# Performance work log

Measured on AMD Instinct MI355X. Metric: run time of the kernel, lower is better.

The kernel has to match this reference:

```python
import jax, jax.numpy as jnp
import numpy as np

EMB = 1024
HID = 1024
VOCAB = 32000
SEQ = 128


def _lstm_cell(x, h, c, W_ih, W_hh, b_ih, b_hh):
    # PyTorch gate order: input, forget, cell(g), output
    gates = x @ W_ih.T + b_ih + h @ W_hh.T + b_hh  # [4H]
    i, f, g, o = jnp.split(gates, 4)
    c_new = jax.nn.sigmoid(f) * c + jax.nn.sigmoid(i) * jnp.tanh(g)
    h_new = jax.nn.sigmoid(o) * jnp.tanh(c_new)
    return h_new, c_new


def setup_inputs() -> dict:
    key = jax.random.key(0)
    ks = jax.random.split(key, 12)
    s_emb = 0.02
    s_lstm = 1.0 / np.sqrt(HID)
    return {
        "sentence": jax.random.randint(ks[0], (SEQ,), 0, VOCAB),
        "given_num": 64,
        "emb": jax.random.normal(ks[1], (VOCAB, EMB), jnp.float32) * s_emb,
        "W_ih_lstm": jax.random.normal(ks[2], (4 * HID, EMB), jnp.float32) * s_lstm,
        "W_hh_lstm": jax.random.normal(ks[3], (4 * HID, HID), jnp.float32) * s_lstm,
        "b_ih_lstm": jax.random.normal(ks[4], (4 * HID,), jnp.float32) * s_lstm,
        "b_hh_lstm": jax.random.normal(ks[5], (4 * HID,), jnp.float32) * s_lstm,
        "W_ih_cell": jax.random.normal(ks[6], (4 * HID, EMB), jnp.float32) * s_lstm,
        "W_hh_cell": jax.random.normal(ks[7], (4 * HID, HID), jnp.float32) * s_lstm,
        "b_ih_cell": jax.random.normal(ks[8], (4 * HID,), jnp.float32) * s_lstm,
        "b_hh_cell": jax.random.normal(ks[9], (4 * HID,), jnp.float32) * s_lstm,
        "W_tag": jax.random.normal(ks[10], (VOCAB, HID), jnp.float32) * s_lstm,
        "b_tag": jax.random.normal(ks[11], (VOCAB,), jnp.float32) * s_lstm,
    }


def reference(sentence, given_num, emb, W_ih_lstm, W_hh_lstm, b_ih_lstm, b_hh_lstm,
              W_ih_cell, W_hh_cell, b_ih_cell, b_hh_cell, W_tag, b_tag):
    given_num = int(given_num)  # static (batch-1 rollout, fixed split point)

    # ---- teacher-forced prefix through nn.LSTM (init_hidden -> zeros) ----
    embeds_existing = emb[sentence[:given_num]]  # [g, E]

    def prefix_step(carry, x):
        h, c = carry
        h, c = _lstm_cell(x, h, c, W_ih_lstm, W_hh_lstm, b_ih_lstm, b_hh_lstm)
        return (h, c), h

    h0 = jnp.zeros((HID,), embeds_existing.dtype)
    (h, c), lstm_out = jax.lax.scan(prefix_step, (h0, h0), embeds_existing)
    tag_prefix = lstm_out @ W_tag.T + b_tag  # [g, V]

    # multinomial over softmax(tag) == categorical over logits; only last row's
    # sample is consumed as x_t
    skeys = jax.random.split(jax.random.key(123), SEQ - given_num + 1)
    x_t = jax.random.categorical(skeys[0], tag_prefix[-1])

    def rollout_step(carry, k):
        x_t, h, c = carry
        e = emb[x_t]
        h, c = _lstm_cell(e, h, c, W_ih_cell, W_hh_cell, b_ih_cell, b_hh_cell)
        logits = h @ W_tag.T + b_tag  # [V]
        x_next = jax.random.categorical(k, logits)
        return (x_next, h, c), logits

    _, tag_roll = jax.lax.scan(rollout_step, (x_t, h, c), skeys[1:])  # [S-g, V]

    tag_space = jnp.concatenate([tag_prefix, tag_roll], axis=0)  # [S, V]
    return jax.nn.log_softmax(tag_space, axis=-1)
```

## Files before the change

kernel.cpp:

```cpp
#include <hip/hip_runtime.h>
#include <cstdint>
#include <cstddef>

#define EMBD 1024
#define HIDD 1024
#define G4   4096
#define VOC  32000
#define SEQL 128
#define GN   64
#define NR   64

#define JAX_PARTITIONABLE 1

__device__ __forceinline__ uint32_t rotl32(uint32_t v, int d) { return (v << d) | (v >> (32 - d)); }

__device__ inline void threefry2x32(uint32_t k0, uint32_t k1, uint32_t x0, uint32_t x1,
                                    uint32_t& o0, uint32_t& o1) {
  uint32_t ks2 = k0 ^ k1 ^ 0x1BD11BDAu;
#define TF_ROUND(r) { x0 += x1; x1 = rotl32(x1, r); x1 ^= x0; }
  x0 += k0;  x1 += k1;
  TF_ROUND(13) TF_ROUND(15) TF_ROUND(26) TF_ROUND(6)
  x0 += k1;  x1 += ks2 + 1u;
  TF_ROUND(17) TF_ROUND(29) TF_ROUND(16) TF_ROUND(24)
  x0 += ks2; x1 += k0 + 2u;
  TF_ROUND(13) TF_ROUND(15) TF_ROUND(26) TF_ROUND(6)
  x0 += k0;  x1 += k1 + 3u;
  TF_ROUND(17) TF_ROUND(29) TF_ROUND(16) TF_ROUND(24)
  x0 += k1;  x1 += ks2 + 4u;
  TF_ROUND(13) TF_ROUND(15) TF_ROUND(26) TF_ROUND(6)
  x0 += ks2; x1 += k0 + 5u;
#undef TF_ROUND
  o0 = x0; o1 = x1;
}

__device__ inline uint32_t rng_bits(uint32_t k0, uint32_t k1, uint32_t idx) {
#if JAX_PARTITIONABLE
  uint32_t h0, h1; threefry2x32(k0, k1, 0u, idx, h0, h1);
  return h0 ^ h1;
#else
  uint32_t h0, h1;
  if (idx < (VOC / 2)) { threefry2x32(k0, k1, idx, idx + (VOC / 2), h0, h1); return h0; }
  else                 { threefry2x32(k0, k1, idx - (VOC / 2), idx, h0, h1); return h1; }
#endif
}

__device__ inline float gumbel_of(uint32_t k0, uint32_t k1, uint32_t idx) {
  uint32_t bits = rng_bits(k0, k1, idx);
  float u = __uint_as_float((bits >> 9) | 0x3f800000u) - 1.0f;
  u = fmaxf(u, 1.17549435e-38f);
  return -logf(-logf(u));
}

__device__ inline unsigned long long packCand(float v, int idx) {
  uint32_t u = __float_as_uint(v);
  u = (u & 0x80000000u) ? ~u : (u | 0x80000000u);
  return ((unsigned long long)u << 32) | (unsigned long long)(0xFFFFFFFFu - (uint32_t)idx);
}

__device__ inline float sigf(float x) { return 1.0f / (1.0f + expf(-x)); }

__global__ void k_init(uint2* keys, unsigned* counters, float* cbuf, float* h0) {
  int t = threadIdx.x;
#if JAX_PARTITIONABLE
  if (t < NR + 1) {
    uint32_t a, b; threefry2x32(0u, 123u, 0u, (uint32_t)t, a, b);
    keys[t] = make_uint2(a, b);
  }
#else
  __shared__ uint32_t buf[2 * (NR + 1)];
  if (t < NR + 1) {
    uint32_t a, b; threefry2x32(0u, 123u, (uint32_t)t, (uint32_t)(t + NR + 1), a, b);
    buf[t] = a; buf[t + NR + 1] = b;
  }
  __syncthreads();
  if (t < NR + 1) keys[t] = make_uint2(buf[2 * t], buf[2 * t + 1]);
#endif
  for (int i = t; i < 66; i += 256) counters[i] = 0u;
  for (int i = t; i < HIDD; i += 256) { cbuf[i] = 0.0f; h0[i] = 0.0f; }
}

__global__ void k_gather(const float* __restrict__ emb, const int* __restrict__ sent,
                         float* __restrict__ X) {
  int m = blockIdx.x;
  int row = sent[m];
  const float4* s = (const float4*)(emb + (size_t)row * EMBD);
  float4* d = (float4*)(X + (size_t)m * EMBD);
  d[threadIdx.x] = s[threadIdx.x];
}

__global__ __launch_bounds__(256) void k_gemm64(const float* __restrict__ A,
                                                const float* __restrict__ B,
                                                const float* __restrict__ bias,
                                                float* __restrict__ C, int ldc) {
  __shared__ float As[64][33];
  __shared__ float Bs[64][33];
  int n0 = blockIdx.x * 64;
  int tn = threadIdx.x & 15, tm = threadIdx.x >> 4;
  float acc[4][4] = {{0.f}};
  for (int k0 = 0; k0 < 1024; k0 += 32) {
    for (int f = threadIdx.x; f < 512; f += 256) {
      int r = f >> 3, c4 = (f & 7) << 2;
      float4 v = *(const float4*)(A + (size_t)r * 1024 + k0 + c4);
      As[r][c4 + 0] = v.x; As[r][c4 + 1] = v.y; As[r][c4 + 2] = v.z; As[r][c4 + 3] = v.w;
      float4 u = *(const float4*)(B + (size_t)(n0 + r) * 1024 + k0 + c4);
      Bs[r][c4 + 0] = u.x; Bs[r][c4 + 1] = u.y; Bs[r][c4 + 2] = u.z; Bs[r][c4 + 3] = u.w;
    }
    __syncthreads();
#pragma unroll
    for (int kk = 0; kk < 32; ++kk) {
      float a0 = As[tm * 4 + 0][kk], a1 = As[tm * 4 + 1][kk];
      float a2 = As[tm * 4 + 2][kk], a3 = As[tm * 4 + 3][kk];
      float b0 = Bs[tn * 4 + 0][kk], b1 = Bs[tn * 4 + 1][kk];
      float b2 = Bs[tn * 4 + 2][kk], b3 = Bs[tn * 4 + 3][kk];
      acc[0][0] += a0 * b0; acc[0][1] += a0 * b1; acc[0][2] += a0 * b2; acc[0][3] += a0 * b3;
      acc[1][0] += a1 * b0; acc[1][1] += a1 * b1; acc[1][2] += a1 * b2; acc[1][3] += a1 * b3;
      acc[2][0] += a2 * b0; acc[2][1] += a2 * b1; acc[2][2] += a2 * b2; acc[2][3] += a2 * b3;
      acc[3][0] += a3 * b0; acc[3][1] += a3 * b1; acc[3][2] += a3 * b2; acc[3][3] += a3 * b3;
    }
    __syncthreads();
  }
#pragma unroll
  for (int i = 0; i < 4; ++i)
#pragma unroll
    for (int j = 0; j < 4; ++j) {
      int m = tm * 4 + i, n = n0 + tn * 4 + j;
      float r = acc[i][j] + (bias ? bias[n] : 0.0f);
      C[(size_t)m * ldc + n] = r;
    }
}

__global__ __launch_bounds__(256) void k_lstm_pre(const float* __restrict__ Whh,
                                                  const float* __restrict__ bih,
                                                  const float* __restrict__ bhh,
                                                  const float* __restrict__ gx, int t,
                                                  const float* __restrict__ hprev,
                                                  float* __restrict__ cbuf,
                                                  float* __restrict__ hout) {
  __shared__ float gs[4];
  int wave = threadIdx.x >> 6, lane = threadIdx.x & 63;
  int j = blockIdx.x;
  int r = j + (wave << 10);
  const float4* h4 = (const float4*)hprev;
  const float4* w4 = (const float4*)(Whh + (size_t)r * 1024);
  float a = 0.0f;
#pragma unroll
  for (int q = 0; q < 4; ++q) {
    float4 w = w4[lane + (q << 6)];
    float4 h = h4[lane + (q << 6)];
    a += w.x * h.x + w.y * h.y + w.z * h.z + w.w * h.w;
  }
#pragma unroll
  for (int off = 32; off; off >>= 1) a += __shfl_xor(a, off, 64);
  if (lane == 0) gs[wave] = a + gx[(size_t)t * G4 + r] + bih[r] + bhh[r];
  __syncthreads();
  if (threadIdx.x == 0) {
    float gi = gs[0], gf = gs[1], gg = gs[2], go = gs[3];
    float cn = sigf(gf) * cbuf[j] + sigf(gi) * tanhf(gg);
    cbuf[j] = cn;
    hout[j] = sigf(go) * tanhf(cn);
  }
}

__global__ __launch_bounds__(256) void k_lstm_roll(const float* __restrict__ Wih,
                                                   const float* __restrict__ Whh,
                                                   const float* __restrict__ bih,
                                                   const float* __restrict__ bhh,
                                                   const float* __restrict__ emb,
                                                   const int* __restrict__ tok, int t,
                                                   const float* __restrict__ hprev,
                                                   float* __restrict__ cbuf,
                                                   float* __restrict__ hout) {
  __shared__ float gs[4];
  int wave = threadIdx.x >> 6, lane = threadIdx.x & 63;
  int j = blockIdx.x;
  int r = j + (wave << 10);
  int row = tok[t];
  const float4* x4 = (const float4*)(emb + (size_t)row * EMBD);
  const float4* h4 = (const float4*)hprev;
  const float4* wi = (const float4*)(Wih + (size_t)r * 1024);
  const float4* wh = (const float4*)(Whh + (size_t)r * 1024);
  float a = 0.0f;
#pragma unroll
  for (int q = 0; q < 4; ++q) {
    float4 w = wi[lane + (q << 6)];
    float4 x = x4[lane + (q << 6)];
    a += w.x * x.x + w.y * x.y + w.z * x.z + w.w * x.w;
    w = wh[lane + (q << 6)];
    float4 h = h4[lane + (q << 6)];
    a += w.x * h.x + w.y * h.y + w.z * h.z + w.w * h.w;
  }
#pragma unroll
  for (int off = 32; off; off >>= 1) a += __shfl_xor(a, off, 64);
  if (lane == 0) gs[wave] = a + bih[r] + bhh[r];
  __syncthreads();
  if (threadIdx.x == 0) {
    float gi = gs[0], gf = gs[1], gg = gs[2], go = gs[3];
    float cn = sigf(gf) * cbuf[j] + sigf(gi) * tanhf(gg);
    cbuf[j] = cn;
    hout[j] = sigf(go) * tanhf(cn);
  }
}

__global__ __launch_bounds__(256) void k_logits(const float* __restrict__ Wtag,
                                                const float* __restrict__ btag,
                                                const float* __restrict__ h,
                                                float* __restrict__ outrow,
                                                const uint2* __restrict__ keys, int key_idx,
                                                unsigned long long* __restrict__ partials,
                                                unsigned* __restrict__ counter,
                                                int* __restrict__ token_out) {
  __shared__ float sums[64];
  __shared__ unsigned long long red[256];
  __shared__ int amLast;
  int wave = threadIdx.x >> 6, lane = threadIdx.x & 63;
  int r0 = blockIdx.x * 64;
  const float4* h4 = (const float4*)h;
  float4 hv[4];
#pragma unroll
  for (int q = 0; q < 4; ++q) hv[q] = h4[lane + (q << 6)];
  for (int rr = 0; rr < 16; ++rr) {
    int lr = wave * 16 + rr;
    int r = r0 + lr;
    const float4* w4 = (const float4*)(Wtag + (size_t)r * 1024);
    float a = 0.0f;
#pragma unroll
    for (int q = 0; q < 4; ++q) {
      float4 w = w4[lane + (q << 6)];
      a += w.x * hv[q].x + w.y * hv[q].y + w.z * hv[q].z + w.w * hv[q].w;
    }
#pragma unroll
    for (int off = 32; off; off >>= 1) a += __shfl_xor(a, off, 64);
    if (lane == 0) sums[lr] = a;
  }
  __syncthreads();
  unsigned long long best = 0ull;
  if (threadIdx.x < 64) {
    int r = r0 + threadIdx.x;
    float L = sums[threadIdx.x] + btag[r];
    outrow[r] = L;
    uint2 K = keys[key_idx];
    float y = L + gumbel_of(K.x, K.y, (uint32_t)r);
    best = packCand(y, r);
#pragma unroll
    for (int off = 32; off; off >>= 1) {
      unsigned long long o = __shfl_xor(best, off, 64);
      if (o > best) best = o;
    }
    if (threadIdx.x == 0) partials[blockIdx.x] = best;
  }
  __threadfence();
  __syncthreads();
  if (threadIdx.x == 0) amLast = (atomicAdd(counter, 1u) == gridDim.x - 1) ? 1 : 0;
  __syncthreads();
  if (amLast) {
    __threadfence();
    unsigned long long b = 0ull;
    for (int i = threadIdx.x; i < (int)gridDim.x; i += 256) {
      unsigned long long v = *((volatile unsigned long long*)(partials + i));
      if (v > b) b = v;
    }
    red[threadIdx.x] = b;
    __syncthreads();
    for (int s = 128; s; s >>= 1) {
      if (threadIdx.x < s) {
        if (red[threadIdx.x + s] > red[threadIdx.x]) red[threadIdx.x] = red[threadIdx.x + s];
      }
      __syncthreads();
    }
    if (threadIdx.x == 0)
      token_out[0] = (int)(0xFFFFFFFFu - (uint32_t)(red[0] & 0xFFFFFFFFull));
  }
}

__global__ __launch_bounds__(256) void k_sample_row(const float* __restrict__ row,
                                                    const uint2* __restrict__ keys, int key_idx,
                                                    unsigned long long* __restrict__ partials,
                                                    unsigned* __restrict__ counter,
                                                    int* __restrict__ token_out) {
  __shared__ unsigned long long red[256];
  __shared__ int amLast;
  int v = blockIdx.x * 256 + threadIdx.x;
  unsigned long long best = 0ull;
  if (v < VOC) {
    uint2 K = keys[key_idx];
    float y = row[v] + gumbel_of(K.x, K.y, (uint32_t)v);
    best = packCand(y, v);
  }
  red[threadIdx.x] = best;
  __syncthreads();
  for (int s = 128; s; s >>= 1) {
    if (threadIdx.x < s) {
      if (red[threadIdx.x + s] > red[threadIdx.x]) red[threadIdx.x] = red[threadIdx.x + s];
    }
    __syncthreads();
  }
  if (threadIdx.x == 0) partials[blockIdx.x] = red[0];
  __threadfence();
  __syncthreads();
  if (threadIdx.x == 0) amLast = (atomicAdd(counter, 1u) == gridDim.x - 1) ? 1 : 0;
  __syncthreads();
  if (amLast) {
    __threadfence();
    unsigned long long b = 0ull;
    for (int i = threadIdx.x; i < (int)gridDim.x; i += 256) {
      unsigned long long val = *((volatile unsigned long long*)(partials + i));
      if (val > b) b = val;
    }
    red[threadIdx.x] = b;
    __syncthreads();
    for (int s = 128; s; s >>= 1) {
      if (threadIdx.x < s) {
        if (red[threadIdx.x + s] > red[threadIdx.x]) red[threadIdx.x] = red[threadIdx.x + s];
      }
      __syncthreads();
    }
    if (threadIdx.x == 0)
      token_out[0] = (int)(0xFFFFFFFFu - (uint32_t)(red[0] & 0xFFFFFFFFull));
  }
}

__global__ __launch_bounds__(256) void k_logsoftmax(float* __restrict__ C) {
  __shared__ float red[256];
  float* row = C + (size_t)blockIdx.x * VOC;
  float m = -INFINITY;
  for (int i = threadIdx.x; i < VOC; i += 256) m = fmaxf(m, row[i]);
  red[threadIdx.x] = m;
  __syncthreads();
  for (int s = 128; s; s >>= 1) {
    if (threadIdx.x < s) red[threadIdx.x] = fmaxf(red[threadIdx.x], red[threadIdx.x + s]);
    __syncthreads();
  }
  m = red[0];
  __syncthreads();
  float sum = 0.0f;
  for (int i = threadIdx.x; i < VOC; i += 256) sum += expf(row[i] - m);
  red[threadIdx.x] = sum;
  __syncthreads();
  for (int s = 128; s; s >>= 1) {
    if (threadIdx.x < s) red[threadIdx.x] += red[threadIdx.x + s];
    __syncthreads();
  }
  float lse = m + logf(red[0]);
  __syncthreads();
  for (int i = threadIdx.x; i < VOC; i += 256) row[i] = row[i] - lse;
}

extern "C" void kernel_launch(void* const* d_in, const int* in_sizes, int n_in,
                              void* d_out, int out_size, void* d_ws, size_t ws_size,
                              hipStream_t stream) {
  (void)in_sizes; (void)n_in; (void)out_size; (void)ws_size;
  const int*   sent  = (const int*)  d_in[0];
  const float* emb   = (const float*)d_in[2];
  const float* Wih_l = (const float*)d_in[3];
  const float* Whh_l = (const float*)d_in[4];
  const float* bih_l = (const float*)d_in[5];
  const float* bhh_l = (const float*)d_in[6];
  const float* Wih_c = (const float*)d_in[7];
  const float* Whh_c = (const float*)d_in[8];
  const float* bih_c = (const float*)d_in[9];
  const float* bhh_c = (const float*)d_in[10];
  const float* Wtag  = (const float*)d_in[11];
  const float* btag  = (const float*)d_in[12];
  float* out = (float*)d_out;

  char* ws = (char*)d_ws;
  uint2*              keys     = (uint2*)(ws + 0);
  int*                tokens   = (int*)(ws + 1024);
  unsigned*           counters = (unsigned*)(ws + 2048);
  unsigned long long* partials = (unsigned long long*)(ws + 4096);
  float*              cbuf     = (float*)(ws + 8192);
  float*              h0       = (float*)(ws + 12288);
  float*              lstm_out = (float*)(ws + 16384);
  float*              hroll    = (float*)(ws + 16384 + 262144);
  float*              X        = (float*)(ws + 16384 + 2 * 262144);
  float*              gx       = (float*)(ws + 16384 + 3 * 262144);

  k_init<<<1, 256, 0, stream>>>(keys, counters, cbuf, h0);
  k_gather<<<GN, 256, 0, stream>>>(emb, sent, X);
  k_gemm64<<<G4 / 64, 256, 0, stream>>>(X, Wih_l, nullptr, gx, G4);
  for (int t = 0; t < GN; ++t) {
    const float* hp = t ? (lstm_out + (size_t)(t - 1) * HIDD) : h0;
    k_lstm_pre<<<HIDD, 256, 0, stream>>>(Whh_l, bih_l, bhh_l, gx, t, hp, cbuf,
                                         lstm_out + (size_t)t * HIDD);
  }
  k_gemm64<<<VOC / 64, 256, 0, stream>>>(lstm_out, Wtag, btag, out, VOC);
  k_sample_row<<<(VOC + 255) / 256, 256, 0, stream>>>(out + (size_t)(GN - 1) * VOC, keys, 0,
                                                      partials, counters + 64, tokens);
  for (int t = 0; t < NR; ++t) {
    const float* hp = t ? (hroll + (size_t)(t - 1) * HIDD) : (lstm_out + (size_t)(GN - 1) * HIDD);
    k_lstm_roll<<<HIDD, 256, 0, stream>>>(Wih_c, Whh_c, bih_c, bhh_c, emb, tokens, t, hp, cbuf,
                                          hroll + (size_t)t * HIDD);
    k_logits<<<VOC / 64, 256, 0, stream>>>(Wtag, btag, hroll + (size_t)t * HIDD,
                                           out + (size_t)(GN + t) * VOC, keys, 1 + t,
                                           partials, counters + t, tokens + t + 1);
  }
  k_logsoftmax<<<SEQL, 256, 0, stream>>>(out);
}
```

Baseline: 5.319 ms.

## Fuse rollout LSTM cell, logits and sampling into one kernel per step

Each rollout step now runs as a single kernel instead of separate LSTM-cell and logits kernels. The first 256 blocks compute the gate pre-activations and signal completion through an atomic counter. All blocks spin until that counter is full, then each recomputes the cell update redundantly into shared memory and computes its slice of the vocabulary logits, Gumbel sample and argmax reduction. The h/c state is double-buffered across steps. The GEMM tile is also narrowed to 32 columns to launch more blocks; the spin barrier relies on all producer blocks being co-resident on the GPU.

```diff
diff --git a/kernel.cpp b/kernel.cpp
--- a/kernel.cpp
+++ b/kernel.cpp
@@ -9,6 +9,8 @@
 #define SEQL 128
 #define GN   64
 #define NR   64
+#define RGRID 500
+#define PPROD 256
 
 #define JAX_PARTITIONABLE 1
 
@@ -61,21 +63,11 @@
 
 __global__ void k_init(uint2* keys, unsigned* counters, float* cbuf, float* h0) {
   int t = threadIdx.x;
-#if JAX_PARTITIONABLE
   if (t < NR + 1) {
     uint32_t a, b; threefry2x32(0u, 123u, 0u, (uint32_t)t, a, b);
     keys[t] = make_uint2(a, b);
   }
-#else
-  __shared__ uint32_t buf[2 * (NR + 1)];
-  if (t < NR + 1) {
-    uint32_t a, b; threefry2x32(0u, 123u, (uint32_t)t, (uint32_t)(t + NR + 1), a, b);
-    buf[t] = a; buf[t + NR + 1] = b;
-  }
-  __syncthreads();
-  if (t < NR + 1) keys[t] = make_uint2(buf[2 * t], buf[2 * t + 1]);
-#endif
-  for (int i = t; i < 66; i += 256) counters[i] = 0u;
+  if (t < 192) counters[t] = 0u;
   for (int i = t; i < HIDD; i += 256) { cbuf[i] = 0.0f; h0[i] = 0.0f; }
 }
 
@@ -88,20 +80,24 @@
   d[threadIdx.x] = s[threadIdx.x];
 }
 
-__global__ __launch_bounds__(256) void k_gemm64(const float* __restrict__ A,
-                                                const float* __restrict__ B,
-                                                const float* __restrict__ bias,
-                                                float* __restrict__ C, int ldc) {
+__global__ __launch_bounds__(256) void k_gemm_n32(const float* __restrict__ A,
+                                                  const float* __restrict__ B,
+                                                  const float* __restrict__ bias,
+                                                  float* __restrict__ C, int ldc) {
   __shared__ float As[64][33];
-  __shared__ float Bs[64][33];
-  int n0 = blockIdx.x * 64;
+  __shared__ float Bs[32][33];
+  int n0 = blockIdx.x * 32;
   int tn = threadIdx.x & 15, tm = threadIdx.x >> 4;
-  float acc[4][4] = {{0.f}};
+  float acc[4][2] = {{0.f}};
   for (int k0 = 0; k0 < 1024; k0 += 32) {
     for (int f = threadIdx.x; f < 512; f += 256) {
       int r = f >> 3, c4 = (f & 7) << 2;
       float4 v = *(const float4*)(A + (size_t)r * 1024 + k0 + c4);
       As[r][c4 + 0] = v.x; As[r][c4 + 1] = v.y; As[r][c4 + 2] = v.z; As[r][c4 + 3] = v.w;
+    }
+    {
+      int f = threadIdx.x;
+      int r = f >> 3, c4 = (f & 7) << 2;
       float4 u = *(const float4*)(B + (size_t)(n0 + r) * 1024 + k0 + c4);
       Bs[r][c4 + 0] = u.x; Bs[r][c4 + 1] = u.y; Bs[r][c4 + 2] = u.z; Bs[r][c4 + 3] = u.w;
     }
@@ -110,22 +106,20 @@
     for (int kk = 0; kk < 32; ++kk) {
       float a0 = As[tm * 4 + 0][kk], a1 = As[tm * 4 + 1][kk];
       float a2 = As[tm * 4 + 2][kk], a3 = As[tm * 4 + 3][kk];
-      float b0 = Bs[tn * 4 + 0][kk], b1 = Bs[tn * 4 + 1][kk];
-      float b2 = Bs[tn * 4 + 2][kk], b3 = Bs[tn * 4 + 3][kk];
-      acc[0][0] += a0 * b0; acc[0][1] += a0 * b1; acc[0][2] += a0 * b2; acc[0][3] += a0 * b3;
-      acc[1][0] += a1 * b0; acc[1][1] += a1 * b1; acc[1][2] += a1 * b2; acc[1][3] += a1 * b3;
-      acc[2][0] += a2 * b0; acc[2][1] += a2 * b1; acc[2][2] += a2 * b2; acc[2][3] += a2 * b3;
-      acc[3][0] += a3 * b0; acc[3][1] += a3 * b1; acc[3][2] += a3 * b2; acc[3][3] += a3 * b3;
+      float b0 = Bs[tn * 2 + 0][kk], b1 = Bs[tn * 2 + 1][kk];
+      acc[0][0] += a0 * b0; acc[0][1] += a0 * b1;
+      acc[1][0] += a1 * b0; acc[1][1] += a1 * b1;
+      acc[2][0] += a2 * b0; acc[2][1] += a2 * b1;
+      acc[3][0] += a3 * b0; acc[3][1] += a3 * b1;
     }
     __syncthreads();
   }
 #pragma unroll
   for (int i = 0; i < 4; ++i)
 #pragma unroll
-    for (int j = 0; j < 4; ++j) {
-      int m = tm * 4 + i, n = n0 + tn * 4 + j;
-      float r = acc[i][j] + (bias ? bias[n] : 0.0f);
-      C[(size_t)m * ldc + n] = r;
+    for (int j = 0; j < 2; ++j) {
+      int m = tm * 4 + i, n = n0 + tn * 2 + j;
+      C[(size_t)m * ldc + n] = acc[i][j] + (bias ? bias[n] : 0.0f);
     }
 }
 
@@ -161,117 +155,6 @@
   }
 }
 
-__global__ __launch_bounds__(256) void k_lstm_roll(const float* __restrict__ Wih,
-                                                   const float* __restrict__ Whh,
-                                                   const float* __restrict__ bih,
-                                                   const float* __restrict__ bhh,
-                                                   const float* __restrict__ emb,
-                                                   const int* __restrict__ tok, int t,
-                                                   const float* __restrict__ hprev,
-                                                   float* __restrict__ cbuf,
-                                                   float* __restrict__ hout) {
-  __shared__ float gs[4];
-  int wave = threadIdx.x >> 6, lane = threadIdx.x & 63;
-  int j = blockIdx.x;
-  int r = j + (wave << 10);
-  int row = tok[t];
-  const float4* x4 = (const float4*)(emb + (size_t)row * EMBD);
-  const float4* h4 = (const float4*)hprev;
-  const float4* wi = (const float4*)(Wih + (size_t)r * 1024);
-  const float4* wh = (const float4*)(Whh + (size_t)r * 1024);
-  float a = 0.0f;
-#pragma unroll
-  for (int q = 0; q < 4; ++q) {
-    float4 w = wi[lane + (q << 6)];
-    float4 x = x4[lane + (q << 6)];
-    a += w.x * x.x + w.y * x.y + w.z * x.z + w.w * x.w;
-    w = wh[lane + (q << 6)];
-    float4 h = h4[lane + (q << 6)];
-    a += w.x * h.x + w.y * h.y + w.z * h.z + w.w * h.w;
-  }
-#pragma unroll
-  for (int off = 32; off; off >>= 1) a += __shfl_xor(a, off, 64);
-  if (lane == 0) gs[wave] = a + bih[r] + bhh[r];
-  __syncthreads();
-  if (threadIdx.x == 0) {
-    float gi = gs[0], gf = gs[1], gg = gs[2], go = gs[3];
-    float cn = sigf(gf) * cbuf[j] + sigf(gi) * tanhf(gg);
-    cbuf[j] = cn;
-    hout[j] = sigf(go) * tanhf(cn);
-  }
-}
-
-__global__ __launch_bounds__(256) void k_logits(const float* __restrict__ Wtag,
-                                                const float* __restrict__ btag,
-                                                const float* __restrict__ h,
-                                                float* __restrict__ outrow,
-                                                const uint2* __restrict__ keys, int key_idx,
-                                                unsigned long long* __restrict__ partials,
-                                                unsigned* __restrict__ counter,
-                                                int* __restrict__ token_out) {
-  __shared__ float sums[64];
-  __shared__ unsigned long long red[256];
-  __shared__ int amLast;
-  int wave = threadIdx.x >> 6, lane = threadIdx.x & 63;
-  int r0 = blockIdx.x * 64;
-  const float4* h4 = (const float4*)h;
-  float4 hv[4];
-#pragma unroll
-  for (int q = 0; q < 4; ++q) hv[q] = h4[lane + (q << 6)];
-  for (int rr = 0; rr < 16; ++rr) {
-    int lr = wave * 16 + rr;
-    int r = r0 + lr;
-    const float4* w4 = (const float4*)(Wtag + (size_t)r * 1024);
-    float a = 0.0f;
-#pragma unroll
-    for (int q = 0; q < 4; ++q) {
-      float4 w = w4[lane + (q << 6)];
-      a += w.x * hv[q].x + w.y * hv[q].y + w.z * hv[q].z + w.w * hv[q].w;
-    }
-#pragma unroll
-    for (int off = 32; off; off >>= 1) a += __shfl_xor(a, off, 64);
-    if (lane == 0) sums[lr] = a;
-  }
-  __syncthreads();
-  unsigned long long best = 0ull;
-  if (threadIdx.x < 64) {
-    int r = r0 + threadIdx.x;
-    float L = sums[threadIdx.x] + btag[r];
-    outrow[r] = L;
-    uint2 K = keys[key_idx];
-    float y = L + gumbel_of(K.x, K.y, (uint32_t)r);
-    best = packCand(y, r);
-#pragma unroll
-    for (int off = 32; off; off >>= 1) {
-      unsigned long long o = __shfl_xor(best, off, 64);
-      if (o > best) best = o;
-    }
-    if (threadIdx.x == 0) partials[blockIdx.x] = best;
-  }
-  __threadfence();
-  __syncthreads();
-  if (threadIdx.x == 0) amLast = (atomicAdd(counter, 1u) == gridDim.x - 1) ? 1 : 0;
-  __syncthreads();
-  if (amLast) {
-    __threadfence();
-    unsigned long long b = 0ull;
-    for (int i = threadIdx.x; i < (int)gridDim.x; i += 256) {
-      unsigned long long v = *((volatile unsigned long long*)(partials + i));
-      if (v > b) b = v;
-    }
-    red[threadIdx.x] = b;
-    __syncthreads();
-    for (int s = 128; s; s >>= 1) {
-      if (threadIdx.x < s) {
-        if (red[threadIdx.x + s] > red[threadIdx.x]) red[threadIdx.x] = red[threadIdx.x + s];
-      }
-      __syncthreads();
-    }
-    if (threadIdx.x == 0)
-      token_out[0] = (int)(0xFFFFFFFFu - (uint32_t)(red[0] & 0xFFFFFFFFull));
-  }
-}
-
 __global__ __launch_bounds__(256) void k_sample_row(const float* __restrict__ row,
                                                     const uint2* __restrict__ keys, int key_idx,
                                                     unsigned long long* __restrict__ partials,
@@ -289,9 +172,7 @@
   red[threadIdx.x] = best;
   __syncthreads();
   for (int s = 128; s; s >>= 1) {
-    if (threadIdx.x < s) {
-      if (red[threadIdx.x + s] > red[threadIdx.x]) red[threadIdx.x] = red[threadIdx.x + s];
-    }
+    if (threadIdx.x < s && red[threadIdx.x + s] > red[threadIdx.x]) red[threadIdx.x] = red[threadIdx.x + s];
     __syncthreads();
   }
   if (threadIdx.x == 0) partials[blockIdx.x] = red[0];
@@ -303,18 +184,144 @@
     __threadfence();
     unsigned long long b = 0ull;
     for (int i = threadIdx.x; i < (int)gridDim.x; i += 256) {
-      unsigned long long val = *((volatile unsigned long long*)(partials + i));
+      unsigned long long val = __hip_atomic_load(partials + i, __ATOMIC_RELAXED, __HIP_MEMORY_SCOPE_AGENT);
       if (val > b) b = val;
     }
     red[threadIdx.x] = b;
     __syncthreads();
     for (int s = 128; s; s >>= 1) {
-      if (threadIdx.x < s) {
-        if (red[threadIdx.x + s] > red[threadIdx.x]) red[threadIdx.x] = red[threadIdx.x + s];
+      if (threadIdx.x < s && red[threadIdx.x + s] > red[threadIdx.x]) red[threadIdx.x] = red[threadIdx.x + s];
+      __syncthreads();
+    }
+    if (threadIdx.x == 0)
+      token_out[0] = (int)(0xFFFFFFFFu - (uint32_t)(red[0] & 0xFFFFFFFFull));
+  }
+}
+
+__global__ __launch_bounds__(256) void k_roll_step(const float* __restrict__ Wih,
+                                                   const float* __restrict__ Whh,
+                                                   const float* __restrict__ bih,
+                                                   const float* __restrict__ bhh,
+                                                   const float* __restrict__ emb,
+                                                   const float* __restrict__ Wtag,
+                                                   const float* __restrict__ btag,
+                                                   const int* __restrict__ tok_in,
+                                                   const float* __restrict__ hprev,
+                                                   const float* __restrict__ cprev,
+                                                   float* __restrict__ hnext,
+                                                   float* __restrict__ cnext,
+                                                   float* __restrict__ gates,
+                                                   unsigned* __restrict__ gate_ctr,
+                                                   const uint2* __restrict__ keys, int key_idx,
+                                                   float* __restrict__ outrow,
+                                                   unsigned long long* __restrict__ partials,
+                                                   unsigned* __restrict__ red_ctr,
+                                                   int* __restrict__ token_out) {
+  __shared__ __align__(16) float hS[1024];
+  __shared__ unsigned long long bw[4];
+  __shared__ unsigned long long red[256];
+  __shared__ int amLast;
+  int tid = threadIdx.x, wave = tid >> 6, lane = tid & 63;
+
+  if (blockIdx.x < PPROD) {
+    int tok = tok_in[0];
+    const float4* x4 = (const float4*)(emb + (size_t)tok * EMBD);
+    const float4* h4 = (const float4*)hprev;
+#pragma unroll
+    for (int rr = 0; rr < 4; ++rr) {
+      int row = blockIdx.x * 16 + wave * 4 + rr;
+      const float4* wi4 = (const float4*)(Wih + (size_t)row * 1024);
+      const float4* wh4 = (const float4*)(Whh + (size_t)row * 1024);
+      float a = 0.0f;
+#pragma unroll
+      for (int q = 0; q < 4; ++q) {
+        float4 w = wi4[lane + (q << 6)];
+        float4 x = x4[lane + (q << 6)];
+        a += w.x * x.x + w.y * x.y + w.z * x.z + w.w * x.w;
+        w = wh4[lane + (q << 6)];
+        float4 h = h4[lane + (q << 6)];
+        a += w.x * h.x + w.y * h.y + w.z * h.z + w.w * h.w;
       }
+#pragma unroll
+      for (int off = 32; off; off >>= 1) a += __shfl_xor(a, off, 64);
+      if (lane == 0) gates[row] = a + bih[row] + bhh[row];
+    }
+  }
+  __syncthreads();
+  if (blockIdx.x < PPROD && tid == 0) {
+    __threadfence();
+    __hip_atomic_fetch_add(gate_ctr, 1u, __ATOMIC_RELEASE, __HIP_MEMORY_SCOPE_AGENT);
+  }
+
+  if (tid == 0) {
+    while (__hip_atomic_load(gate_ctr, __ATOMIC_ACQUIRE, __HIP_MEMORY_SCOPE_AGENT) < (unsigned)PPROD)
+      __builtin_amdgcn_s_sleep(1);
+  }
+  __syncthreads();
+
+  for (int j = tid; j < 1024; j += 256) {
+    float gi = __hip_atomic_load(gates + j,        __ATOMIC_RELAXED, __HIP_MEMORY_SCOPE_AGENT);
+    float gf = __hip_atomic_load(gates + j + 1024, __ATOMIC_RELAXED, __HIP_MEMORY_SCOPE_AGENT);
+    float gg = __hip_atomic_load(gates + j + 2048, __ATOMIC_RELAXED, __HIP_MEMORY_SCOPE_AGENT);
+    float go = __hip_atomic_load(gates + j + 3072, __ATOMIC_RELAXED, __HIP_MEMORY_SCOPE_AGENT);
+    float cn = sigf(gf) * cprev[j] + sigf(gi) * tanhf(gg);
+    float hn = sigf(go) * tanhf(cn);
+    hS[j] = hn;
+    if (blockIdx.x == 0) { cnext[j] = cn; hnext[j] = hn; }
+  }
+  __syncthreads();
+
+  float4 hv[4];
+#pragma unroll
+  for (int q = 0; q < 4; ++q) hv[q] = ((const float4*)hS)[lane + (q << 6)];
+  unsigned long long wbest = 0ull;
+  uint2 K = keys[key_idx];
+  int r0 = blockIdx.x * 64;
+  for (int rr = 0; rr < 16; ++rr) {
+    int row = r0 + wave * 16 + rr;
+    const float4* w4 = (const float4*)(Wtag + (size_t)row * 1024);
+    float acc = 0.0f;
+#pragma unroll
+    for (int q = 0; q < 4; ++q) {
+      float4 w = w4[lane + (q << 6)];
+      acc += w.x * hv[q].x + w.y * hv[q].y + w.z * hv[q].z + w.w * hv[q].w;
+    }
+#pragma unroll
+    for (int off = 32; off; off >>= 1) acc += __shfl_xor(acc, off, 64);
+    if (lane == 0) {
+      float L = acc + btag[row];
+      outrow[row] = L;
+      float y = L + gumbel_of(K.x, K.y, (uint32_t)row);
+      unsigned long long c = packCand(y, row);
+      if (c > wbest) wbest = c;
+    }
+  }
+  if (lane == 0) bw[wave] = wbest;
+  __syncthreads();
+  if (tid == 0) {
+    unsigned long long b = bw[0];
+#pragma unroll
+    for (int w = 1; w < 4; ++w) if (bw[w] > b) b = bw[w];
+    partials[blockIdx.x] = b;
+  }
+  __threadfence();
+  __syncthreads();
+  if (tid == 0) amLast = (atomicAdd(red_ctr, 1u) == gridDim.x - 1) ? 1 : 0;
+  __syncthreads();
+  if (amLast) {
+    __threadfence();
+    unsigned long long b = 0ull;
+    for (int i = tid; i < (int)gridDim.x; i += 256) {
+      unsigned long long v = __hip_atomic_load(partials + i, __ATOMIC_RELAXED, __HIP_MEMORY_SCOPE_AGENT);
+      if (v > b) b = v;
+    }
+    red[tid] = b;
+    __syncthreads();
+    for (int s = 128; s; s >>= 1) {
+      if (tid < s && red[tid + s] > red[tid]) red[tid] = red[tid + s];
       __syncthreads();
     }
-    if (threadIdx.x == 0)
+    if (tid == 0)
       token_out[0] = (int)(0xFFFFFFFFu - (uint32_t)(red[0] & 0xFFFFFFFFull));
   }
 }
@@ -368,31 +375,42 @@
   int*                tokens   = (int*)(ws + 1024);
   unsigned*           counters = (unsigned*)(ws + 2048);
   unsigned long long* partials = (unsigned long long*)(ws + 4096);
-  float*              cbuf     = (float*)(ws + 8192);
+  float*              cbuf_pre = (float*)(ws + 8192);
   float*              h0       = (float*)(ws + 12288);
-  float*              lstm_out = (float*)(ws + 16384);
-  float*              hroll    = (float*)(ws + 16384 + 262144);
-  float*              X        = (float*)(ws + 16384 + 2 * 262144);
-  float*              gx       = (float*)(ws + 16384 + 3 * 262144);
-
-  k_init<<<1, 256, 0, stream>>>(keys, counters, cbuf, h0);
+  float*              gbuf     = (float*)(ws + 16384);
+  float*              croll    = (float*)(ws + 49152);
+  float*              hroll    = (float*)(ws + 57344);
+  float*              lstm_out = (float*)(ws + 65536);
+  float*              X        = (float*)(ws + 65536 + 262144);
+  float*              gx       = (float*)(ws + 65536 + 2*262144);
+
+  k_init<<<1, 256, 0, stream>>>(keys, counters, cbuf_pre, h0);
   k_gather<<<GN, 256, 0, stream>>>(emb, sent, X);
-  k_gemm64<<<G4 / 64, 256, 0, stream>>>(X, Wih_l, nullptr, gx, G4);
+  k_gemm_n32<<<G4 / 32, 256, 0, stream>>>(X, Wih_l, nullptr, gx, G4);
+
   for (int t = 0; t < GN; ++t) {
     const float* hp = t ? (lstm_out + (size_t)(t - 1) * HIDD) : h0;
-    k_lstm_pre<<<HIDD, 256, 0, stream>>>(Whh_l, bih_l, bhh_l, gx, t, hp, cbuf,
+    k_lstm_pre<<<HIDD, 256, 0, stream>>>(Whh_l, bih_l, bhh_l, gx, t, hp, cbuf_pre,
                                          lstm_out + (size_t)t * HIDD);
   }
-  k_gemm64<<<VOC / 64, 256, 0, stream>>>(lstm_out, Wtag, btag, out, VOC);
+
+  k_gemm_n32<<<VOC / 32, 256, 0, stream>>>(lstm_out, Wtag, btag, out, VOC);
+
   k_sample_row<<<(VOC + 255) / 256, 256, 0, stream>>>(out + (size_t)(GN - 1) * VOC, keys, 0,
-                                                      partials, counters + 64, tokens);
+                                                      partials, counters + 128, tokens);
+
   for (int t = 0; t < NR; ++t) {
-    const float* hp = t ? (hroll + (size_t)(t - 1) * HIDD) : (lstm_out + (size_t)(GN - 1) * HIDD);
-    k_lstm_roll<<<HIDD, 256, 0, stream>>>(Wih_c, Whh_c, bih_c, bhh_c, emb, tokens, t, hp, cbuf,
-                                          hroll + (size_t)t * HIDD);
-    k_logits<<<VOC / 64, 256, 0, stream>>>(Wtag, btag, hroll + (size_t)t * HIDD,
-                                           out + (size_t)(GN + t) * VOC, keys, 1 + t,
-                                           partials, counters + t, tokens + t + 1);
-  }
+    const float* hp = t ? (hroll + (size_t)(t & 1) * HIDD) : (lstm_out + (size_t)(GN - 1) * HIDD);
+    const float* cp = t ? (croll + (size_t)(t & 1) * HIDD) : cbuf_pre;
+    float* hn = hroll + (size_t)((t + 1) & 1) * HIDD;
+    float* cn = croll + (size_t)((t + 1) & 1) * HIDD;
+    float* g  = gbuf + (size_t)(t & 1) * G4;
+    k_roll_step<<<RGRID, 256, 0, stream>>>(Wih_c, Whh_c, bih_c, bhh_c, emb, Wtag, btag,
+                                           tokens + t, hp, cp, hn, cn, g,
+                                           counters + t, keys, 1 + t,
+                                           out + (size_t)(GN + t) * VOC,
+                                           partials, counters + 64 + t, tokens + t + 1);
+  }
+
   k_logsoftmax<<<SEQL, 256, 0, stream>>>(out);
 }
```

Measured after the change: 9.815 ms. +84.5%, slower.
